# Optimization experiments

Hardware: AMD Instinct MI355X
Metric: run time of the kernel (lower is better)

## Reference

```python
import jax, jax.numpy as jnp
import numpy as np

B, S, D = 4, 2048, 512
H, Dh = 8, 64  # head_dim(=num heads)=8, qkv_dim(per-head)=64
SCALE = 1.0 / float(np.sqrt(Dh))


def setup_inputs() -> dict:
    key = jax.random.key(0)
    ks = jax.random.split(key, 11)
    w = 1.0 / float(np.sqrt(D))
    return {
        "x": jax.random.normal(ks[0], (B, S, D), dtype=jnp.float32),
        "mask": jax.random.randint(ks[1], (B, 1, S, S), 0, 2, dtype=jnp.int32),
        "Wq": jax.random.normal(ks[2], (D, H * Dh), dtype=jnp.float32) * w,
        "bq": jax.random.normal(ks[3], (H * Dh,), dtype=jnp.float32) * w,
        "Wk": jax.random.normal(ks[4], (D, H * Dh), dtype=jnp.float32) * w,
        "bk": jax.random.normal(ks[5], (H * Dh,), dtype=jnp.float32) * w,
        "Wv": jax.random.normal(ks[6], (D, H * Dh), dtype=jnp.float32) * w,
        "bv": jax.random.normal(ks[7], (H * Dh,), dtype=jnp.float32) * w,
        "Wo": jax.random.normal(ks[8], (H * Dh, D), dtype=jnp.float32) * w,
        "bo": jax.random.normal(ks[9], (D,), dtype=jnp.float32) * w,
    }


def reference(x, mask, Wq, bq, Wk, bk, Wv, bv, Wo, bo):
    b = x.shape[0]
    q = (x @ Wq + bq).reshape(b, S, H, Dh)
    k = (x @ Wk + bk).reshape(b, S, H, Dh)
    v = (x @ Wv + bv).reshape(b, S, H, Dh)
    # [b,h,q,k] attention scores, softmax over k
    score = jax.nn.softmax(jnp.einsum('bqhd,bkhd->bhqk', q, k) * SCALE, axis=-1)
    # faithful quirk: mask applied AFTER softmax, masked entries set to 1e-20
    score = jnp.where(mask == 1, jnp.float32(1e-20), score)
    # faithful quirk: einsum 'bvhd,bhqk->bvhd' sums score over q AND k -> [b,h] scalar per head
    s = score.sum(axis=(-2, -1))  # [b, h]
    att = v * s[:, None, :, None]  # [b, S, H, Dh]
    out = att.reshape(b, S, H * Dh) @ Wo + bo
    return out
```

## Files before the change

### kernel.cpp

```cpp
#include <hip/hip_runtime.h>
#include <cstdint>
#include <cstddef>

#define DEVINL __device__ __forceinline__

constexpr int S_ = 2048;
constexpr int D_ = 512;
constexpr int H_ = 8;
constexpr float SCALE_ = 0.125f;
constexpr float SCALE_L2E_ = 0.18033688011112f;

using short8 = __attribute__((ext_vector_type(8))) short;
using f32x4  = __attribute__((ext_vector_type(4))) float;

DEVINL unsigned short f2bf(float f){
  unsigned u = __builtin_bit_cast(unsigned, f);
  u += 0x7FFFu + ((u >> 16) & 1u);
  return (unsigned short)(u >> 16);
}
DEVINL float bf2f(unsigned short h){
  return __builtin_bit_cast(float, ((unsigned)h) << 16);
}

DEVINL float fast_exp2(float x){ return __builtin_amdgcn_exp2f(x); }

DEVINL void gload16(const void* g, void* l){
  __builtin_amdgcn_global_load_lds(
      (__attribute__((address_space(1))) void*)(g),
      (__attribute__((address_space(3))) void*)(l), 16, 0, 0);
}

__global__ void cast_x_kernel(const float* __restrict__ x, unsigned short* __restrict__ xb){
  int i = blockIdx.x * 256 + threadIdx.x;
  const float* p = x + (size_t)i * 8;
  float4 a = *(const float4*)p;
  float4 b = *(const float4*)(p + 4);
  short8 o;
  o[0]=f2bf(a.x); o[1]=f2bf(a.y); o[2]=f2bf(a.z); o[3]=f2bf(a.w);
  o[4]=f2bf(b.x); o[5]=f2bf(b.y); o[6]=f2bf(b.z); o[7]=f2bf(b.w);
  *(short8*)(xb + (size_t)i*8) = o;
}

__global__ void mask_bits_kernel(const int* __restrict__ mask, unsigned char* __restrict__ bits){
  unsigned tid = blockIdx.x * 256 + threadIdx.x;
  #pragma unroll
  for (int it = 0; it < 4; ++it){
    size_t bidx = (size_t)tid + (size_t)it * 524288;
    const int* p = mask + bidx * 8;
    int4 a = *(const int4*)p;
    int4 c = *(const int4*)(p + 4);
    unsigned v = (unsigned)(a.x != 0)       | ((unsigned)(a.y != 0) << 1)
               | ((unsigned)(a.z != 0) << 2) | ((unsigned)(a.w != 0) << 3)
               | ((unsigned)(c.x != 0) << 4) | ((unsigned)(c.y != 0) << 5)
               | ((unsigned)(c.z != 0) << 6) | ((unsigned)(c.w != 0) << 7);
    bits[bidx] = (unsigned char)v;
  }
}

__global__ void castT_kernel(const float* __restrict__ W0, const float* __restrict__ W1,
                             const float* __restrict__ W2, const float* __restrict__ W3,
                             unsigned short* __restrict__ WT){
  __shared__ float tile[32][33];
  const int z = blockIdx.z;
  const float* W = (z==0) ? W0 : (z==1 ? W1 : (z==2 ? W2 : W3));
  const float scale = (z==0) ? SCALE_L2E_ : 1.0f;
  unsigned short* out = WT + (size_t)z * D_ * D_;
  int n0 = blockIdx.x*32, k0 = blockIdx.y*32;
  int tx = threadIdx.x, ty = threadIdx.y;
  #pragma unroll
  for (int j=0;j<4;j++)
    tile[ty+j*8][tx] = W[(size_t)(k0+ty+j*8)*D_ + n0+tx];
  __syncthreads();
  #pragma unroll
  for (int j=0;j<4;j++)
    out[(size_t)(n0+ty+j*8)*D_ + k0+tx] = f2bf(tile[tx][ty+j*8]*scale);
}

template<typename OutT>
__global__ __launch_bounds__(256) void gemm_bt(
    const unsigned short* __restrict__ A, long long Az,
    const unsigned short* __restrict__ BT, long long Bz,
    const float* __restrict__ bias0, const float* __restrict__ bias1, const float* __restrict__ bias2,
    float bs0, float bs1, float bs2,
    OutT* __restrict__ Cp, long long Cz)
{
  __shared__ unsigned short As[128*64];
  __shared__ unsigned short Bs[128*64];
  const int z = blockIdx.z;
  const unsigned short* Ab = A + (size_t)z*Az;
  const unsigned short* Bb = BT + (size_t)z*Bz;
  const float* bias = (z==0) ? bias0 : (z==1 ? bias1 : bias2);
  const float bscale = (z==0) ? bs0 : (z==1 ? bs1 : bs2);
  OutT* C = Cp + (size_t)z*Cz;
  const int m0 = blockIdx.y*128, n0 = blockIdx.x*128;
  const int t = threadIdx.x, lane = t & 63, w = t >> 6;
  const int wr = w >> 1, wc = w & 1;
  const int g = lane >> 4, lq = lane & 15;
  f32x4 acc[4][4] = {};
  for (int kk = 0; kk < D_; kk += 64){
    #pragma unroll
    for (int p = 0; p < 4; p++){
      int o = p*4096 + t*16;
      int row = o >> 7;
      int cb  = o & 127;
      int scb = cb ^ ((row & 7) << 4);
      gload16((const char*)Ab + ((size_t)(m0+row)*D_ + kk)*2 + scb, (char*)As + o);
      gload16((const char*)Bb + ((size_t)(n0+row)*D_ + kk)*2 + scb, (char*)Bs + o);
    }
    __syncthreads();
    #pragma unroll
    for (int ks = 0; ks < 2; ks++){
      short8 af[4], bf[4];
      #pragma unroll
      for (int i = 0; i < 4; i++){
        int rowA = wr*64 + i*16 + lq;
        af[i] = *(const short8*)((const char*)As + ((rowA*128 + ks*64 + g*16) ^ ((rowA&7)<<4)));
        int rowB = wc*64 + i*16 + lq;
        bf[i] = *(const short8*)((const char*)Bs + ((rowB*128 + ks*64 + g*16) ^ ((rowB&7)<<4)));
      }
      #pragma unroll
      for (int i = 0; i < 4; i++)
        #pragma unroll
        for (int j = 0; j < 4; j++)
          acc[i][j] = __builtin_amdgcn_mfma_f32_16x16x32_bf16(af[i], bf[j], acc[i][j], 0, 0, 0);
    }
    __syncthreads();
  }
  #pragma unroll
  for (int i = 0; i < 4; i++){
    #pragma unroll
    for (int j = 0; j < 4; j++){
      int col = n0 + wc*64 + j*16 + lq;
      float bvv = bias[col]*bscale;
      #pragma unroll
      for (int r = 0; r < 4; r++){
        int row = m0 + wr*64 + i*16 + g*4 + r;
        float v = acc[i][j][r] + bvv;
        if constexpr (sizeof(OutT) == 4) C[(size_t)row*D_ + col] = (OutT)v;
        else                             C[(size_t)row*D_ + col] = (OutT)f2bf(v);
      }
    }
  }
}

__global__ __launch_bounds__(512) void attn_zm_kernel(
    const unsigned short* __restrict__ Q, const unsigned short* __restrict__ Kg,
    const unsigned* __restrict__ bitsW, float* __restrict__ Zb, float* __restrict__ Mb)
{
  const int qt = blockIdx.x, kz = blockIdx.y, b = blockIdx.z;
  const int t = threadIdx.x, lane = t & 63, h = t >> 6;
  const int g = lane >> 4, lq = lane & 15;
  const int qbase = qt * 64;

  unsigned wb[4][8];
  #pragma unroll
  for (int qs = 0; qs < 4; qs++){
    const uint4* wp = (const uint4*)(bitsW + ((size_t)(b*S_ + qbase + qs*16 + lq))*(S_/32) + kz*8);
    uint4 wA = wp[0], wB = wp[1];
    wb[qs][0]=wA.x; wb[qs][1]=wA.y; wb[qs][2]=wA.z; wb[qs][3]=wA.w;
    wb[qs][4]=wB.x; wb[qs][5]=wB.y; wb[qs][6]=wB.z; wb[qs][7]=wB.w;
  }

  short8 qf[4][2];
  #pragma unroll
  for (int qs = 0; qs < 4; qs++)
    #pragma unroll
    for (int c = 0; c < 2; c++)
      qf[qs][c] = *(const short8*)(Q + ((size_t)(b*S_ + qbase + qs*16 + lq))*D_ + h*64 + c*32 + g*8);

  const unsigned short* Kbase = Kg + ((size_t)(b*S_ + kz*256))*D_ + h*64 + g*8;

  float Z[4], Mm[4];
  #pragma unroll
  for (int qs = 0; qs < 4; qs++){ Z[qs] = 0.f; Mm[qs] = 0.f; }

  #pragma unroll
  for (int kt2 = 0; kt2 < 8; ++kt2){
    const unsigned short* Kr = Kbase + (size_t)kt2*32*D_;
    #pragma unroll
    for (int ks = 0; ks < 2; ks++){
      short8 A0 = *(const short8*)(Kr + (ks*16+lq)*D_);
      short8 A1 = *(const short8*)(Kr + (ks*16+lq)*D_ + 32);
      #pragma unroll
      for (int qs = 0; qs < 4; qs++){
        f32x4 d = {0.f,0.f,0.f,0.f};
        d = __builtin_amdgcn_mfma_f32_16x16x32_bf16(A0, qf[qs][0], d, 0, 0, 0);
        d = __builtin_amdgcn_mfma_f32_16x16x32_bf16(A1, qf[qs][1], d, 0, 0, 0);
        unsigned nib = wb[qs][kt2] >> (ks*16 + g*4);
        #pragma unroll
        for (int r = 0; r < 4; r++){
          float p = fast_exp2(d[r]);
          Z[qs] += p;
          Mm[qs] = fmaf((float)((nib >> r) & 1u), p, Mm[qs]);
        }
      }
    }
  }
  #pragma unroll
  for (int qs = 0; qs < 4; qs++){
    Z[qs]  += __shfl_xor(Z[qs], 16);  Mm[qs] += __shfl_xor(Mm[qs], 16);
    Z[qs]  += __shfl_xor(Z[qs], 32);  Mm[qs] += __shfl_xor(Mm[qs], 32);
  }
  if (g == 0){
    int base = (b*H_ + h)*S_ + qbase + lq;
    #pragma unroll
    for (int qs = 0; qs < 4; qs++){
      atomicAdd(&Zb[base + qs*16], Z[qs]);
      atomicAdd(&Mb[base + qs*16], Mm[qs]);
    }
  }
}

__global__ __launch_bounds__(256) void finalize_s(const float* __restrict__ Zb,
                                                  const float* __restrict__ Mb,
                                                  float* __restrict__ sbh){
  const int bh = blockIdx.x;
  const int t = threadIdx.x;
  const float* Z = Zb + (size_t)bh*S_;
  const float* M = Mb + (size_t)bh*S_;
  float acc = 0.f;
  #pragma unroll
  for (int q = t; q < S_; q += 256){
    float z = Z[q];
    acc += (z - M[q]) / z;
  }
  #pragma unroll
  for (int m = 1; m < 64; m <<= 1) acc += __shfl_xor(acc, m);
  __shared__ float wsum[4];
  if ((t & 63) == 0) wsum[t >> 6] = acc;
  __syncthreads();
  if (t == 0) sbh[bh] = wsum[0] + wsum[1] + wsum[2] + wsum[3];
}

__global__ void scale_woT_kernel(const unsigned short* __restrict__ WoT,
                                 const float* __restrict__ sbh,
                                 unsigned short* __restrict__ outw){
  int i = blockIdx.x*256 + threadIdx.x;
  size_t e = (size_t)i * 8;
  int k = (int)(e & 511);
  int n = (int)((e >> 9) & 511);
  int b = (int)(e >> 18);
  float sv = sbh[b*H_ + (k >> 6)];
  short8 wv = *(const short8*)(WoT + (size_t)n*D_ + k);
  short8 o;
  #pragma unroll
  for (int j = 0; j < 8; j++) o[j] = (short)f2bf(bf2f((unsigned short)wv[j]) * sv);
  *(short8*)(outw + e) = o;
}

extern "C" void kernel_launch(void* const* d_in, const int* in_sizes, int n_in,
                              void* d_out, int out_size, void* d_ws, size_t ws_size,
                              hipStream_t stream) {
  (void)in_sizes; (void)n_in; (void)out_size; (void)ws_size;
  const float* x  = (const float*)d_in[0];
  const int* mask = (const int*)d_in[1];
  const float* Wq = (const float*)d_in[2];
  const float* bq = (const float*)d_in[3];
  const float* Wk = (const float*)d_in[4];
  const float* bk = (const float*)d_in[5];
  const float* Wv = (const float*)d_in[6];
  const float* bv = (const float*)d_in[7];
  const float* Wo = (const float*)d_in[8];
  const float* bo = (const float*)d_in[9];
  float* out = (float*)d_out;

  char* ws = (char*)d_ws;
  unsigned short* xb   = (unsigned short*)(ws);
  unsigned short* wT   = (unsigned short*)(ws +  8388608);
  unsigned short* woT  = (unsigned short*)(ws +  9961472);
  unsigned short* Qb   = (unsigned short*)(ws + 10485760);
  unsigned short* Kb   = (unsigned short*)(ws + 18874368);
  unsigned short* Vb   = (unsigned short*)(ws + 27262976);
  unsigned short* woST = (unsigned short*)(ws + 35651584);
  float*          sbh  = (float*)         (ws + 37748736);
  float*          Zbuf = (float*)(ws);
  float*          Mbuf = (float*)(ws + 262144);
  unsigned char*  bits = (unsigned char*)(ws + 35651584);

  cast_x_kernel<<<2048, 256, 0, stream>>>(x, xb);
  castT_kernel<<<dim3(16,16,4), dim3(32,8), 0, stream>>>(Wq, Wk, Wv, Wo, wT);
  mask_bits_kernel<<<2048, 256, 0, stream>>>(mask, bits);

  gemm_bt<unsigned short><<<dim3(4,64,3), 256, 0, stream>>>(
      xb, 0LL, wT, 262144LL, bq, bk, bv, SCALE_L2E_, 1.0f, 1.0f, Qb, 4194304LL);

  hipMemsetAsync(Zbuf, 0, 524288, stream);

  attn_zm_kernel<<<dim3(32,8,4), 512, 0, stream>>>(Qb, Kb, (const unsigned*)bits, Zbuf, Mbuf);
  finalize_s<<<32, 256, 0, stream>>>(Zbuf, Mbuf, sbh);

  scale_woT_kernel<<<512, 256, 0, stream>>>(woT, sbh, woST);

  gemm_bt<float><<<dim3(4,16,4), 256, 0, stream>>>(
      Vb, 1048576LL, woST, 262144LL, bo, bo, bo, 1.0f, 1.0f, 1.0f, out, 1048576LL);
}
```

Baseline: 121.1 us.

## Software-pipeline K and mask loads in attention Z/M kernel, split heads across blocks

The attention partial-sum kernel now prefetches K fragments two steps ahead and mask words one tile ahead in rotating register buffers, instead of loading all mask bits up front and K inline. It also splits the 8 heads into two blocks of 4 waves (256 threads, grid z doubled) with a 4-blocks-per-CU launch bound. Accumulation switches to per-lane vector Z/M with a reduction at the end. The aim is to hide global load latency behind MFMA and exp work and to raise occupancy. The cost is more register pressure from the prefetch buffers and Q fragments being loaded in more blocks.

New measurement: 181.6 us. 49.9% more time.

```diff
diff --git a/kernel.cpp b/kernel.cpp
--- a/kernel.cpp
+++ b/kernel.cpp
@@ -143,23 +143,16 @@
   }
 }
 
-__global__ __launch_bounds__(512) void attn_zm_kernel(
+__global__ __launch_bounds__(256, 4) void attn_zm_kernel(
     const unsigned short* __restrict__ Q, const unsigned short* __restrict__ Kg,
     const unsigned* __restrict__ bitsW, float* __restrict__ Zb, float* __restrict__ Mb)
 {
-  const int qt = blockIdx.x, kz = blockIdx.y, b = blockIdx.z;
-  const int t = threadIdx.x, lane = t & 63, h = t >> 6;
-  const int g = lane >> 4, lq = lane & 15;
+  const int qt = blockIdx.x, kz = blockIdx.y, zz = blockIdx.z;
+  const int b = zz >> 1, hg = zz & 1;
+  const int t = threadIdx.x, lane = t & 63;
+  const int h = hg*4 + (t >> 6);
+  const int g = lane >> 4, lq = lane & 15, g4 = g*4;
   const int qbase = qt * 64;
-
-  unsigned wb[4][8];
-  #pragma unroll
-  for (int qs = 0; qs < 4; qs++){
-    const uint4* wp = (const uint4*)(bitsW + ((size_t)(b*S_ + qbase + qs*16 + lq))*(S_/32) + kz*8);
-    uint4 wA = wp[0], wB = wp[1];
-    wb[qs][0]=wA.x; wb[qs][1]=wA.y; wb[qs][2]=wA.z; wb[qs][3]=wA.w;
-    wb[qs][4]=wB.x; wb[qs][5]=wB.y; wb[qs][6]=wB.z; wb[qs][7]=wB.w;
-  }
 
   short8 qf[4][2];
   #pragma unroll
@@ -169,44 +162,63 @@
       qf[qs][c] = *(const short8*)(Q + ((size_t)(b*S_ + qbase + qs*16 + lq))*D_ + h*64 + c*32 + g*8);
 
   const unsigned short* Kbase = Kg + ((size_t)(b*S_ + kz*256))*D_ + h*64 + g*8;
-
-  float Z[4], Mm[4];
-  #pragma unroll
-  for (int qs = 0; qs < 4; qs++){ Z[qs] = 0.f; Mm[qs] = 0.f; }
-
-  #pragma unroll
-  for (int kt2 = 0; kt2 < 8; ++kt2){
-    const unsigned short* Kr = Kbase + (size_t)kt2*32*D_;
-    #pragma unroll
-    for (int ks = 0; ks < 2; ks++){
-      short8 A0 = *(const short8*)(Kr + (ks*16+lq)*D_);
-      short8 A1 = *(const short8*)(Kr + (ks*16+lq)*D_ + 32);
+  const unsigned* wbase = bitsW + ((size_t)(b*S_ + qbase + lq))*(S_/32) + kz*8;
+
+  f32x4 Z4[4], M4[4];
+  #pragma unroll
+  for (int qs = 0; qs < 4; qs++){
+    Z4[qs] = (f32x4){0.f,0.f,0.f,0.f};
+    M4[qs] = (f32x4){0.f,0.f,0.f,0.f};
+  }
+
+  short8  Ab[4][2];
+  unsigned mwb[2][4];
+
+#define LDA(i) { const unsigned short* r_ = Kbase + (size_t)((i)*16+lq)*D_;            \
+                 Ab[(i)&3][0] = *(const short8*)r_;                                     \
+                 Ab[(i)&3][1] = *(const short8*)(r_+32); }
+#define LDM(k2) { mwb[(k2)&1][0] = wbase[0*1024 + (k2)];                                \
+                  mwb[(k2)&1][1] = wbase[1*1024 + (k2)];                                \
+                  mwb[(k2)&1][2] = wbase[2*1024 + (k2)];                                \
+                  mwb[(k2)&1][3] = wbase[3*1024 + (k2)]; }
+
+  LDA(0); LDA(1);
+  LDM(0); LDM(1);
+
+  #pragma unroll
+  for (int i = 0; i < 16; ++i){
+    const int kt2 = i >> 1, ks = i & 1;
+    if (i + 2 < 16) LDA(i+2);
+    #pragma unroll
+    for (int qs = 0; qs < 4; qs++){
+      f32x4 d = (f32x4){0.f,0.f,0.f,0.f};
+      d = __builtin_amdgcn_mfma_f32_16x16x32_bf16(Ab[i&3][0], qf[qs][0], d, 0, 0, 0);
+      d = __builtin_amdgcn_mfma_f32_16x16x32_bf16(Ab[i&3][1], qf[qs][1], d, 0, 0, 0);
+      unsigned nib = mwb[kt2&1][qs] >> (ks*16 + g4);
+      f32x4 p, mf;
       #pragma unroll
-      for (int qs = 0; qs < 4; qs++){
-        f32x4 d = {0.f,0.f,0.f,0.f};
-        d = __builtin_amdgcn_mfma_f32_16x16x32_bf16(A0, qf[qs][0], d, 0, 0, 0);
-        d = __builtin_amdgcn_mfma_f32_16x16x32_bf16(A1, qf[qs][1], d, 0, 0, 0);
-        unsigned nib = wb[qs][kt2] >> (ks*16 + g*4);
-        #pragma unroll
-        for (int r = 0; r < 4; r++){
-          float p = fast_exp2(d[r]);
-          Z[qs] += p;
-          Mm[qs] = fmaf((float)((nib >> r) & 1u), p, Mm[qs]);
-        }
+      for (int r = 0; r < 4; r++){
+        p[r]  = fast_exp2(d[r]);
+        mf[r] = (float)((nib >> r) & 1u);
       }
-    }
-  }
+      Z4[qs] += p;
+      M4[qs] += mf * p;
+    }
+    if (ks == 1 && kt2 + 2 < 8) LDM(kt2+2);
+  }
+#undef LDA
+#undef LDM
+
   #pragma unroll
   for (int qs = 0; qs < 4; qs++){
-    Z[qs]  += __shfl_xor(Z[qs], 16);  Mm[qs] += __shfl_xor(Mm[qs], 16);
-    Z[qs]  += __shfl_xor(Z[qs], 32);  Mm[qs] += __shfl_xor(Mm[qs], 32);
-  }
-  if (g == 0){
-    int base = (b*H_ + h)*S_ + qbase + lq;
-    #pragma unroll
-    for (int qs = 0; qs < 4; qs++){
-      atomicAdd(&Zb[base + qs*16], Z[qs]);
-      atomicAdd(&Mb[base + qs*16], Mm[qs]);
+    float z = (Z4[qs][0] + Z4[qs][1]) + (Z4[qs][2] + Z4[qs][3]);
+    float m = (M4[qs][0] + M4[qs][1]) + (M4[qs][2] + M4[qs][3]);
+    z += __shfl_xor(z, 16);  m += __shfl_xor(m, 16);
+    z += __shfl_xor(z, 32);  m += __shfl_xor(m, 32);
+    if (g == 0){
+      int base = (b*H_ + h)*S_ + qbase + qs*16 + lq;
+      atomicAdd(&Zb[base], z);
+      atomicAdd(&Mb[base], m);
     }
   }
 }
@@ -286,7 +298,7 @@
 
   hipMemsetAsync(Zbuf, 0, 524288, stream);
 
-  attn_zm_kernel<<<dim3(32,8,4), 512, 0, stream>>>(Qb, Kb, (const unsigned*)bits, Zbuf, Mbuf);
+  attn_zm_kernel<<<dim3(32,8,8), 256, 0, stream>>>(Qb, Kb, (const unsigned*)bits, Zbuf, Mbuf);
   finalize_s<<<32, 256, 0, stream>>>(Zbuf, Mbuf, sbh);
 
   scale_woT_kernel<<<512, 256, 0, stream>>>(woT, sbh, woST);
```
